# Kernel tuning notes

Measured on AMD Instinct MI355X. Metric: run time of the kernel, lower is better.

The kernel has to match this reference:

```python
import jax, jax.numpy as jnp
import numpy as np

FP16_MAX = 65504.0  # clamp_fp16 bound
GROUP = 64          # SVDQuant int4 group size along in_features


def _int4_quant_dequant(w):
    """Symmetric per-(out_channel, group) int4 fake-quant of a weight [out, in].
    Emulates the W4 weight numerics of SVDQW4A4Linear at the dequantized level."""
    o, i = w.shape
    wg = w.reshape(o, i // GROUP, GROUP)
    scale = np.max(np.abs(wg), axis=-1, keepdims=True) / 7.0
    scale = np.where(scale == 0.0, 1.0, scale)
    q = np.clip(np.round(wg / scale), -8, 7)
    return (q * scale).reshape(o, i).astype(np.float32)


def setup_inputs() -> dict:
    dim, hidden = 3072, 8192
    B, S = 2, 4096
    rng = np.random.default_rng(0)
    # fused [w1; w3] weight: [2*hidden, dim]; down proj w2: [dim, hidden]
    w13 = _int4_quant_dequant((rng.standard_normal((2 * hidden, dim)) * 0.02).astype(np.float32))
    w2 = _int4_quant_dequant((rng.standard_normal((dim, hidden)) * 0.02).astype(np.float32))
    key = jax.random.key(0)
    x = jax.random.normal(key, (B, S, dim), dtype=jnp.float32)
    return {"x": x, "w13": jnp.asarray(w13), "w2": jnp.asarray(w2)}


def reference(x, w13, w2):
    # fused gate/up projection: [B,S,dim] @ [2H,dim]^T -> [B,S,2H]
    h = jnp.einsum("bsd,hd->bsh", x, w13)
    # NOTE: original code does `x3, x1 = x.chunk(2, dim=-1)` -> first half is x3
    x3, x1 = jnp.split(h, 2, axis=-1)
    g = jnp.clip(jax.nn.silu(x1) * x3, -FP16_MAX, FP16_MAX)  # clamp_fp16
    # down projection: [B,S,H] @ [dim,H]^T -> [B,S,dim]
    return jnp.einsum("bsh,dh->bsd", g, w2)
```

## Files before the change

### kernel.cpp

```cpp
#include <hip/hip_runtime.h>
#include <hip/hip_bf16.h>


typedef __attribute__((ext_vector_type(8))) __bf16 bf16x8;
typedef __attribute__((ext_vector_type(4))) float f32x4;

#define GLD_LDS16(gptr, lptr)                                                        \
  __builtin_amdgcn_global_load_lds(                                                  \
      (const __attribute__((address_space(1))) void*)(gptr),                         \
      (__attribute__((address_space(3))) void*)(lptr), 16, 0, 0)

__device__ __forceinline__ __bf16 bfr(float f) {
  unsigned int u = __builtin_bit_cast(unsigned int, f);
  unsigned short r = (unsigned short)((u + 0x7FFFu + ((u >> 16) & 1u)) >> 16);
  return __builtin_bit_cast(__bf16, r);
}

__global__ __launch_bounds__(256)
void k_cvt(const float* __restrict__ src, unsigned short* __restrict__ dst, long n) {
  long i = ((long)blockIdx.x * 256 + threadIdx.x) * 8;
  const long stride = (long)gridDim.x * 256 * 8;
  for (; i < n; i += stride) {
    float4 f0 = *(const float4*)(src + i);
    float4 f1 = *(const float4*)(src + i + 4);
    bf16x8 o;
    o[0] = bfr(f0.x); o[1] = bfr(f0.y); o[2] = bfr(f0.z); o[3] = bfr(f0.w);
    o[4] = bfr(f1.x); o[5] = bfr(f1.y); o[6] = bfr(f1.z); o[7] = bfr(f1.w);
    *(bf16x8*)(dst + i) = o;
  }
}

__device__ __forceinline__ void stage_f32_tile(const float* __restrict__ src, int ld,
                                               unsigned short* __restrict__ lds, int t) {
  const int srow = t >> 3;
  const int sg = t & 7;
#pragma unroll
  for (int c = 0; c < 4; ++c) {
    const int row = c * 32 + srow;
    const float* p = src + (size_t)row * ld + sg * 8;
    float4 f0 = *(const float4*)p;
    float4 f1 = *(const float4*)(p + 4);
    bf16x8 o;
    o[0] = bfr(f0.x); o[1] = bfr(f0.y); o[2] = bfr(f0.z); o[3] = bfr(f0.w);
    o[4] = bfr(f1.x); o[5] = bfr(f1.y); o[6] = bfr(f1.z); o[7] = bfr(f1.w);
    *(bf16x8*)(lds + row * 64 + ((sg ^ (row & 7)) * 8)) = o;
  }
}

__global__ __launch_bounds__(256, 2)
void k_gateup_f(const unsigned short* __restrict__ X,
                const unsigned short* __restrict__ W13,
                __hip_bfloat16* __restrict__ G)
{
  constexpr int K = 3072;
  constexpr int LDG = 8192;
  __shared__ unsigned short As[128 * 64];
  __shared__ unsigned short B3s[128 * 64];
  __shared__ unsigned short B1s[128 * 64];

  const int t = threadIdx.x;
  const int lane = t & 63;
  const int wid = t >> 6;
  const int wm = wid >> 1, wn = wid & 1;
  const int l15 = lane & 15, lhi = lane >> 4;
  const int nb = blockIdx.x, mb = blockIdx.y;

  const int srow = t >> 3;
  const int scol = ((t & 7) ^ (srow & 7)) * 8;
  const unsigned short* xa  = X   + (size_t)(mb * 128 + srow) * K + scol;
  const unsigned short* wb3 = W13 + (size_t)(nb * 128 + srow) * K + scol;
  const unsigned short* wb1 = W13 + (size_t)(8192 + nb * 128 + srow) * K + scol;
  unsigned short* lA  = As  + t * 8;
  unsigned short* lB3 = B3s + t * 8;
  unsigned short* lB1 = B1s + t * 8;

  f32x4 acc3[4][4], acc1[4][4];
#pragma unroll
  for (int i = 0; i < 4; ++i)
#pragma unroll
    for (int j = 0; j < 4; ++j) {
      acc3[i][j] = (f32x4){0.f, 0.f, 0.f, 0.f};
      acc1[i][j] = (f32x4){0.f, 0.f, 0.f, 0.f};
    }
  const int sw = l15 & 7;

  for (int kt = 0; kt < K; kt += 64) {
    __syncthreads();
#pragma unroll
    for (int c = 0; c < 4; ++c) {
      GLD_LDS16(xa  + (size_t)(c * 32) * K + kt, lA  + c * 2048);
      GLD_LDS16(wb3 + (size_t)(c * 32) * K + kt, lB3 + c * 2048);
      GLD_LDS16(wb1 + (size_t)(c * 32) * K + kt, lB1 + c * 2048);
    }
    __syncthreads();
#pragma unroll
    for (int kk = 0; kk < 2; ++kk) {
      const int slot = (kk * 4 + lhi) ^ sw;
      bf16x8 av[4], bv3[4], bv1[4];
#pragma unroll
      for (int i = 0; i < 4; ++i) {
        av[i]  = *(const bf16x8*)(As  + (wm * 64 + i * 16 + l15) * 64 + slot * 8);
        bv3[i] = *(const bf16x8*)(B3s + (wn * 64 + i * 16 + l15) * 64 + slot * 8);
        bv1[i] = *(const bf16x8*)(B1s + (wn * 64 + i * 16 + l15) * 64 + slot * 8);
      }
#pragma unroll
      for (int i = 0; i < 4; ++i)
#pragma unroll
        for (int j = 0; j < 4; ++j) {
          acc3[i][j] = __builtin_amdgcn_mfma_f32_16x16x32_bf16(av[i], bv3[j], acc3[i][j], 0, 0, 0);
          acc1[i][j] = __builtin_amdgcn_mfma_f32_16x16x32_bf16(av[i], bv1[j], acc1[i][j], 0, 0, 0);
        }
    }
  }

  const int gr0 = mb * 128 + wm * 64;
  const int gc0 = nb * 128 + wn * 64;
#pragma unroll
  for (int i = 0; i < 4; ++i)
#pragma unroll
    for (int j = 0; j < 4; ++j)
#pragma unroll
      for (int r = 0; r < 4; ++r) {
        float h3 = acc3[i][j][r];
        float h1 = acc1[i][j][r];
        float s  = h1 / (1.f + __expf(-h1));
        float g  = fminf(fmaxf(s * h3, -65504.f), 65504.f);
        G[(size_t)(gr0 + i * 16 + lhi * 4 + r) * LDG + (gc0 + j * 16 + l15)] =
            __float2bfloat16(g);
      }
}

__global__ __launch_bounds__(256, 2)
void k_gateup_s(const float* __restrict__ X,
                const float* __restrict__ W13,
                __hip_bfloat16* __restrict__ G)
{
  constexpr int K = 3072;
  constexpr int LDG = 8192;
  __shared__ unsigned short As[128 * 64];
  __shared__ unsigned short B3s[128 * 64];
  __shared__ unsigned short B1s[128 * 64];

  const int t = threadIdx.x;
  const int lane = t & 63;
  const int wid = t >> 6;
  const int wm = wid >> 1, wn = wid & 1;
  const int l15 = lane & 15, lhi = lane >> 4;
  const int nb = blockIdx.x, mb = blockIdx.y;

  const float* xa  = X   + (size_t)(mb * 128) * K;
  const float* wb3 = W13 + (size_t)(nb * 128) * K;
  const float* wb1 = W13 + (size_t)(8192 + nb * 128) * K;

  f32x4 acc3[4][4], acc1[4][4];
#pragma unroll
  for (int i = 0; i < 4; ++i)
#pragma unroll
    for (int j = 0; j < 4; ++j) {
      acc3[i][j] = (f32x4){0.f, 0.f, 0.f, 0.f};
      acc1[i][j] = (f32x4){0.f, 0.f, 0.f, 0.f};
    }
  const int sw = l15 & 7;

  for (int kt = 0; kt < K; kt += 64) {
    __syncthreads();
    stage_f32_tile(xa  + kt, K, As,  t);
    stage_f32_tile(wb3 + kt, K, B3s, t);
    stage_f32_tile(wb1 + kt, K, B1s, t);
    __syncthreads();
#pragma unroll
    for (int kk = 0; kk < 2; ++kk) {
      const int slot = (kk * 4 + lhi) ^ sw;
      bf16x8 av[4], bv3[4], bv1[4];
#pragma unroll
      for (int i = 0; i < 4; ++i) {
        av[i]  = *(const bf16x8*)(As  + (wm * 64 + i * 16 + l15) * 64 + slot * 8);
        bv3[i] = *(const bf16x8*)(B3s + (wn * 64 + i * 16 + l15) * 64 + slot * 8);
        bv1[i] = *(const bf16x8*)(B1s + (wn * 64 + i * 16 + l15) * 64 + slot * 8);
      }
#pragma unroll
      for (int i = 0; i < 4; ++i)
#pragma unroll
        for (int j = 0; j < 4; ++j) {
          acc3[i][j] = __builtin_amdgcn_mfma_f32_16x16x32_bf16(av[i], bv3[j], acc3[i][j], 0, 0, 0);
          acc1[i][j] = __builtin_amdgcn_mfma_f32_16x16x32_bf16(av[i], bv1[j], acc1[i][j], 0, 0, 0);
        }
    }
  }

  const int gr0 = mb * 128 + wm * 64;
  const int gc0 = nb * 128 + wn * 64;
#pragma unroll
  for (int i = 0; i < 4; ++i)
#pragma unroll
    for (int j = 0; j < 4; ++j)
#pragma unroll
      for (int r = 0; r < 4; ++r) {
        float h3 = acc3[i][j][r];
        float h1 = acc1[i][j][r];
        float s  = h1 / (1.f + __expf(-h1));
        float g  = fminf(fmaxf(s * h3, -65504.f), 65504.f);
        G[(size_t)(gr0 + i * 16 + lhi * 4 + r) * LDG + (gc0 + j * 16 + l15)] =
            __float2bfloat16(g);
      }
}

__global__ __launch_bounds__(256, 2)
void k_down_f(const unsigned short* __restrict__ G,
              const unsigned short* __restrict__ W2,
              float* __restrict__ Out)
{
  constexpr int K = 8192;
  constexpr int LDO = 3072;
  __shared__ unsigned short As[128 * 64];
  __shared__ unsigned short Bs[128 * 64];

  const int t = threadIdx.x;
  const int lane = t & 63;
  const int wid = t >> 6;
  const int wm = wid >> 1, wn = wid & 1;
  const int l15 = lane & 15, lhi = lane >> 4;
  const int nb = blockIdx.x, mb = blockIdx.y;

  const int srow = t >> 3;
  const int scol = ((t & 7) ^ (srow & 7)) * 8;
  const unsigned short* ga = G  + (size_t)(mb * 128 + srow) * K + scol;
  const unsigned short* wb = W2 + (size_t)(nb * 128 + srow) * K + scol;
  unsigned short* lA = As + t * 8;
  unsigned short* lB = Bs + t * 8;

  f32x4 acc[4][4];
#pragma unroll
  for (int i = 0; i < 4; ++i)
#pragma unroll
    for (int j = 0; j < 4; ++j)
      acc[i][j] = (f32x4){0.f, 0.f, 0.f, 0.f};
  const int sw = l15 & 7;

  for (int kt = 0; kt < K; kt += 64) {
    __syncthreads();
#pragma unroll
    for (int c = 0; c < 4; ++c) {
      GLD_LDS16(ga + (size_t)(c * 32) * K + kt, lA + c * 2048);
      GLD_LDS16(wb + (size_t)(c * 32) * K + kt, lB + c * 2048);
    }
    __syncthreads();
#pragma unroll
    for (int kk = 0; kk < 2; ++kk) {
      const int slot = (kk * 4 + lhi) ^ sw;
      bf16x8 av[4], bv[4];
#pragma unroll
      for (int i = 0; i < 4; ++i) {
        av[i] = *(const bf16x8*)(As + (wm * 64 + i * 16 + l15) * 64 + slot * 8);
        bv[i] = *(const bf16x8*)(Bs + (wn * 64 + i * 16 + l15) * 64 + slot * 8);
      }
#pragma unroll
      for (int i = 0; i < 4; ++i)
#pragma unroll
        for (int j = 0; j < 4; ++j)
          acc[i][j] = __builtin_amdgcn_mfma_f32_16x16x32_bf16(av[i], bv[j], acc[i][j], 0, 0, 0);
    }
  }

  const int r0 = mb * 128 + wm * 64;
  const int c0 = nb * 128 + wn * 64;
#pragma unroll
  for (int i = 0; i < 4; ++i)
#pragma unroll
    for (int j = 0; j < 4; ++j)
#pragma unroll
      for (int r = 0; r < 4; ++r)
        Out[(size_t)(r0 + i * 16 + lhi * 4 + r) * LDO + (c0 + j * 16 + l15)] =
            acc[i][j][r];
}

__global__ __launch_bounds__(256, 2)
void k_down_s(const unsigned short* __restrict__ G,
              const float* __restrict__ W2,
              float* __restrict__ Out)
{
  constexpr int K = 8192;
  constexpr int LDO = 3072;
  __shared__ unsigned short As[128 * 64];
  __shared__ unsigned short Bs[128 * 64];

  const int t = threadIdx.x;
  const int lane = t & 63;
  const int wid = t >> 6;
  const int wm = wid >> 1, wn = wid & 1;
  const int l15 = lane & 15, lhi = lane >> 4;
  const int nb = blockIdx.x, mb = blockIdx.y;

  const int srow = t >> 3;
  const int scol = ((t & 7) ^ (srow & 7)) * 8;
  const unsigned short* ga = G + (size_t)(mb * 128 + srow) * K + scol;
  const float* wb = W2 + (size_t)(nb * 128) * K;
  unsigned short* lA = As + t * 8;

  f32x4 acc[4][4];
#pragma unroll
  for (int i = 0; i < 4; ++i)
#pragma unroll
    for (int j = 0; j < 4; ++j)
      acc[i][j] = (f32x4){0.f, 0.f, 0.f, 0.f};
  const int sw = l15 & 7;

  for (int kt = 0; kt < K; kt += 64) {
    __syncthreads();
#pragma unroll
    for (int c = 0; c < 4; ++c)
      GLD_LDS16(ga + (size_t)(c * 32) * K + kt, lA + c * 2048);
    stage_f32_tile(wb + kt, K, Bs, t);
    __syncthreads();
#pragma unroll
    for (int kk = 0; kk < 2; ++kk) {
      const int slot = (kk * 4 + lhi) ^ sw;
      bf16x8 av[4], bv[4];
#pragma unroll
      for (int i = 0; i < 4; ++i) {
        av[i] = *(const bf16x8*)(As + (wm * 64 + i * 16 + l15) * 64 + slot * 8);
        bv[i] = *(const bf16x8*)(Bs + (wn * 64 + i * 16 + l15) * 64 + slot * 8);
      }
#pragma unroll
      for (int i = 0; i < 4; ++i)
#pragma unroll
        for (int j = 0; j < 4; ++j)
          acc[i][j] = __builtin_amdgcn_mfma_f32_16x16x32_bf16(av[i], bv[j], acc[i][j], 0, 0, 0);
    }
  }

  const int r0 = mb * 128 + wm * 64;
  const int c0 = nb * 128 + wn * 64;
#pragma unroll
  for (int i = 0; i < 4; ++i)
#pragma unroll
    for (int j = 0; j < 4; ++j)
#pragma unroll
      for (int r = 0; r < 4; ++r)
        Out[(size_t)(r0 + i * 16 + lhi * 4 + r) * LDO + (c0 + j * 16 + l15)] =
            acc[i][j][r];
}

extern "C" void kernel_launch(void* const* d_in, const int* in_sizes, int n_in,
                              void* d_out, int out_size, void* d_ws, size_t ws_size,
                              hipStream_t stream) {
  const float* x   = (const float*)d_in[0];
  const float* w13 = (const float*)d_in[1];
  const float* w2  = (const float*)d_in[2];
  float* out = (float*)d_out;

  const long NX = 25165824L, NW13 = 50331648L, NW2 = 25165824L;
  const size_t XB = 50331648, W13B = 100663296, W2B = 50331648, GB = 134217728;

  if (ws_size >= XB + W13B + W2B + GB) {
    unsigned short* xb   = (unsigned short*)d_ws;
    unsigned short* w13b = (unsigned short*)((char*)d_ws + XB);
    unsigned short* w2b  = (unsigned short*)((char*)d_ws + XB + W13B);
    __hip_bfloat16* g    = (__hip_bfloat16*)((char*)d_ws + XB + W13B + W2B);
    k_cvt<<<2048, 256, 0, stream>>>(x,   xb,   NX);
    k_cvt<<<2048, 256, 0, stream>>>(w13, w13b, NW13);
    k_cvt<<<2048, 256, 0, stream>>>(w2,  w2b,  NW2);
    k_gateup_f<<<dim3(64, 64), dim3(256), 0, stream>>>(xb, w13b, (__hip_bfloat16*)g);
    k_down_f<<<dim3(24, 64), dim3(256), 0, stream>>>((const unsigned short*)g, w2b, out);
  } else {
    long mc = (long)(ws_size / (8192 * 2));
    mc -= mc % 128;
    if (mc > 8192) mc = 8192;
    if (mc < 128) mc = 128;
    for (long m0 = 0; m0 < 8192; m0 += mc) {
      long mrows = 8192 - m0 < mc ? 8192 - m0 : mc;
      __hip_bfloat16* g = (__hip_bfloat16*)d_ws;
      k_gateup_s<<<dim3(64, mrows / 128), dim3(256), 0, stream>>>(
          x + m0 * 3072, w13, g);
      k_down_s<<<dim3(24, mrows / 128), dim3(256), 0, stream>>>(
          (const unsigned short*)g, w2, out + m0 * 3072);
    }
  }
}
```

Measured before the change: 1.234 ms.

## Rewrite GEMM kernels with 256x128 tiles, double-buffered LDS prefetch, and block swizzle

Replaces both GEMM kernels with 512-thread, 8-wave versions that use 256x128 output tiles. Global-to-LDS loads are double-buffered two K-steps ahead, with finer-grained waitcnt and barriers so loads overlap the MFMA work. The kernels also add s_setprio around MFMA bursts and a block-index swizzle for L2 locality. The chunked fallback path for a small workspace is dropped, so the code now assumes a large workspace is always available.

```diff
diff --git a/kernel.cpp b/kernel.cpp
--- a/kernel.cpp
+++ b/kernel.cpp
@@ -9,6 +9,19 @@
   __builtin_amdgcn_global_load_lds(                                                  \
       (const __attribute__((address_space(1))) void*)(gptr),                         \
       (__attribute__((address_space(3))) void*)(lptr), 16, 0, 0)
+
+#define VMCNT(n) asm volatile("s_waitcnt vmcnt(" #n ")" ::: "memory")
+#define BAR_SYNC()                                          \
+  do {                                                      \
+    asm volatile("s_waitcnt lgkmcnt(0)" ::: "memory");      \
+    __builtin_amdgcn_s_barrier();                           \
+    asm volatile("" ::: "memory");                          \
+  } while (0)
+#define BAR_ONLY()                                          \
+  do {                                                      \
+    __builtin_amdgcn_s_barrier();                           \
+    asm volatile("" ::: "memory");                          \
+  } while (0)
 
 __device__ __forceinline__ __bf16 bfr(float f) {
   unsigned int u = __builtin_bit_cast(unsigned int, f);
@@ -30,315 +43,262 @@
   }
 }
 
-__device__ __forceinline__ void stage_f32_tile(const float* __restrict__ src, int ld,
-                                               unsigned short* __restrict__ lds, int t) {
-  const int srow = t >> 3;
-  const int sg = t & 7;
-#pragma unroll
-  for (int c = 0; c < 4; ++c) {
-    const int row = c * 32 + srow;
-    const float* p = src + (size_t)row * ld + sg * 8;
-    float4 f0 = *(const float4*)p;
-    float4 f1 = *(const float4*)(p + 4);
-    bf16x8 o;
-    o[0] = bfr(f0.x); o[1] = bfr(f0.y); o[2] = bfr(f0.z); o[3] = bfr(f0.w);
-    o[4] = bfr(f1.x); o[5] = bfr(f1.y); o[6] = bfr(f1.z); o[7] = bfr(f1.w);
-    *(bf16x8*)(lds + row * 64 + ((sg ^ (row & 7)) * 8)) = o;
-  }
-}
-
-__global__ __launch_bounds__(256, 2)
-void k_gateup_f(const unsigned short* __restrict__ X,
-                const unsigned short* __restrict__ W13,
-                __hip_bfloat16* __restrict__ G)
+__global__ __launch_bounds__(512, 2)
+void k_gateup8(const unsigned short* __restrict__ X,
+               const unsigned short* __restrict__ W13,
+               __hip_bfloat16* __restrict__ G)
 {
-  constexpr int K = 3072;
-  constexpr int LDG = 8192;
-  __shared__ unsigned short As[128 * 64];
-  __shared__ unsigned short B3s[128 * 64];
-  __shared__ unsigned short B1s[128 * 64];
+  constexpr int K = 3072, LDG = 8192, NT = K / 64;
+  __shared__ unsigned short lds[65536];
 
   const int t = threadIdx.x;
-  const int lane = t & 63;
-  const int wid = t >> 6;
-  const int wm = wid >> 1, wn = wid & 1;
-  const int l15 = lane & 15, lhi = lane >> 4;
-  const int nb = blockIdx.x, mb = blockIdx.y;
+  const int lane = t & 63, wid = t >> 6;
+  const int wm = wid >> 2, wn = wid & 3;
+  const int l15 = lane & 15, lhi = lane >> 4, sw = l15 & 7;
+
+  const int bid = blockIdx.x;
+  const int swz = (bid & 7) * 256 + (bid >> 3);
+  const int mb = swz >> 6, nb = swz & 63;
 
   const int srow = t >> 3;
   const int scol = ((t & 7) ^ (srow & 7)) * 8;
-  const unsigned short* xa  = X   + (size_t)(mb * 128 + srow) * K + scol;
-  const unsigned short* wb3 = W13 + (size_t)(nb * 128 + srow) * K + scol;
-  const unsigned short* wb1 = W13 + (size_t)(8192 + nb * 128 + srow) * K + scol;
-  unsigned short* lA  = As  + t * 8;
-  unsigned short* lB3 = B3s + t * 8;
-  unsigned short* lB1 = B1s + t * 8;
-
-  f32x4 acc3[4][4], acc1[4][4];
-#pragma unroll
-  for (int i = 0; i < 4; ++i)
-#pragma unroll
-    for (int j = 0; j < 4; ++j) {
-      acc3[i][j] = (f32x4){0.f, 0.f, 0.f, 0.f};
-      acc1[i][j] = (f32x4){0.f, 0.f, 0.f, 0.f};
-    }
-  const int sw = l15 & 7;
-
-  for (int kt = 0; kt < K; kt += 64) {
-    __syncthreads();
-#pragma unroll
-    for (int c = 0; c < 4; ++c) {
-      GLD_LDS16(xa  + (size_t)(c * 32) * K + kt, lA  + c * 2048);
-      GLD_LDS16(wb3 + (size_t)(c * 32) * K + kt, lB3 + c * 2048);
-      GLD_LDS16(wb1 + (size_t)(c * 32) * K + kt, lB1 + c * 2048);
-    }
-    __syncthreads();
+  const unsigned short* xa = X   + (size_t)(mb * 256 + srow) * K + scol;
+  const unsigned short* b3 = W13 + (size_t)(nb * 128 + srow) * K + scol;
+  const unsigned short* b1 = W13 + (size_t)(8192 + nb * 128 + srow) * K + scol;
+  const int lo = t * 8;
+
+  f32x4 acc3[8][2], acc1[8][2];
+#pragma unroll
+  for (int m = 0; m < 8; ++m)
+#pragma unroll
+    for (int n = 0; n < 2; ++n) {
+      acc3[m][n] = (f32x4){0.f, 0.f, 0.f, 0.f};
+      acc1[m][n] = (f32x4){0.f, 0.f, 0.f, 0.f};
+    }
+
+#pragma unroll
+  for (int tt = 0; tt < 2; ++tt) {
+    unsigned short* A  = lds + tt * 32768;
+    unsigned short* B3 = A + 16384;
+    unsigned short* B1 = A + 24576;
+    const int kt = tt * 64;
+#pragma unroll
+    for (int q = 0; q < 4; ++q)
+      GLD_LDS16(xa + (size_t)(q * 64) * K + kt, A + q * 4096 + lo);
+#pragma unroll
+    for (int r = 0; r < 2; ++r) {
+      GLD_LDS16(b3 + (size_t)(r * 64) * K + kt, B3 + r * 4096 + lo);
+      GLD_LDS16(b1 + (size_t)(r * 64) * K + kt, B1 + r * 4096 + lo);
+    }
+  }
+
+  for (int tk = 0; tk < NT; ++tk) {
+    unsigned short* A  = lds + (tk & 1) * 32768;
+    unsigned short* B3 = A + 16384;
+    unsigned short* B1 = A + 24576;
+    const int ks = (tk + 2 < NT ? tk + 2 : 0) * 64;
+
+    VMCNT(8);
+    BAR_ONLY();
+
+    bf16x8 ra[4][2], r3a[2], r1a[2], r3b[2], r1b[2];
+#pragma unroll
+    for (int m = 0; m < 4; ++m)
+#pragma unroll
+      for (int kk = 0; kk < 2; ++kk)
+        ra[m][kk] = *(const bf16x8*)(A + (wm * 128 + m * 16 + l15) * 64 + ((kk * 4 + lhi) ^ sw) * 8);
 #pragma unroll
     for (int kk = 0; kk < 2; ++kk) {
-      const int slot = (kk * 4 + lhi) ^ sw;
-      bf16x8 av[4], bv3[4], bv1[4];
-#pragma unroll
-      for (int i = 0; i < 4; ++i) {
-        av[i]  = *(const bf16x8*)(As  + (wm * 64 + i * 16 + l15) * 64 + slot * 8);
-        bv3[i] = *(const bf16x8*)(B3s + (wn * 64 + i * 16 + l15) * 64 + slot * 8);
-        bv1[i] = *(const bf16x8*)(B1s + (wn * 64 + i * 16 + l15) * 64 + slot * 8);
-      }
-#pragma unroll
-      for (int i = 0; i < 4; ++i)
-#pragma unroll
-        for (int j = 0; j < 4; ++j) {
-          acc3[i][j] = __builtin_amdgcn_mfma_f32_16x16x32_bf16(av[i], bv3[j], acc3[i][j], 0, 0, 0);
-          acc1[i][j] = __builtin_amdgcn_mfma_f32_16x16x32_bf16(av[i], bv1[j], acc1[i][j], 0, 0, 0);
-        }
-    }
-  }
-
-  const int gr0 = mb * 128 + wm * 64;
-  const int gc0 = nb * 128 + wn * 64;
-#pragma unroll
-  for (int i = 0; i < 4; ++i)
-#pragma unroll
-    for (int j = 0; j < 4; ++j)
+      r3a[kk] = *(const bf16x8*)(B3 + (wn * 32 + l15) * 64 + ((kk * 4 + lhi) ^ sw) * 8);
+      r1a[kk] = *(const bf16x8*)(B1 + (wn * 32 + l15) * 64 + ((kk * 4 + lhi) ^ sw) * 8);
+    }
+    __builtin_amdgcn_s_setprio(1);
+#pragma unroll
+    for (int m = 0; m < 4; ++m)
+#pragma unroll
+      for (int kk = 0; kk < 2; ++kk) {
+        acc3[m][0] = __builtin_amdgcn_mfma_f32_16x16x32_bf16(ra[m][kk], r3a[kk], acc3[m][0], 0, 0, 0);
+        acc1[m][0] = __builtin_amdgcn_mfma_f32_16x16x32_bf16(ra[m][kk], r1a[kk], acc1[m][0], 0, 0, 0);
+      }
+    __builtin_amdgcn_s_setprio(0);
+    BAR_SYNC();
+
+    GLD_LDS16(xa + (size_t)(0 * 64) * K + ks, A + 0 * 4096 + lo);
+    GLD_LDS16(xa + (size_t)(2 * 64) * K + ks, A + 2 * 4096 + lo);
+#pragma unroll
+    for (int kk = 0; kk < 2; ++kk) {
+      r3b[kk] = *(const bf16x8*)(B3 + (wn * 32 + 16 + l15) * 64 + ((kk * 4 + lhi) ^ sw) * 8);
+      r1b[kk] = *(const bf16x8*)(B1 + (wn * 32 + 16 + l15) * 64 + ((kk * 4 + lhi) ^ sw) * 8);
+    }
+    __builtin_amdgcn_s_setprio(1);
+#pragma unroll
+    for (int m = 0; m < 4; ++m)
+#pragma unroll
+      for (int kk = 0; kk < 2; ++kk) {
+        acc3[m][1] = __builtin_amdgcn_mfma_f32_16x16x32_bf16(ra[m][kk], r3b[kk], acc3[m][1], 0, 0, 0);
+        acc1[m][1] = __builtin_amdgcn_mfma_f32_16x16x32_bf16(ra[m][kk], r1b[kk], acc1[m][1], 0, 0, 0);
+      }
+    __builtin_amdgcn_s_setprio(0);
+    BAR_SYNC();
+
+#pragma unroll
+    for (int r = 0; r < 2; ++r) {
+      GLD_LDS16(b3 + (size_t)(r * 64) * K + ks, B3 + r * 4096 + lo);
+      GLD_LDS16(b1 + (size_t)(r * 64) * K + ks, B1 + r * 4096 + lo);
+    }
+#pragma unroll
+    for (int m = 0; m < 4; ++m)
+#pragma unroll
+      for (int kk = 0; kk < 2; ++kk)
+        ra[m][kk] = *(const bf16x8*)(A + (wm * 128 + 64 + m * 16 + l15) * 64 + ((kk * 4 + lhi) ^ sw) * 8);
+    __builtin_amdgcn_s_setprio(1);
+#pragma unroll
+    for (int m = 0; m < 4; ++m)
+#pragma unroll
+      for (int kk = 0; kk < 2; ++kk) {
+        acc3[4 + m][0] = __builtin_amdgcn_mfma_f32_16x16x32_bf16(ra[m][kk], r3a[kk], acc3[4 + m][0], 0, 0, 0);
+        acc1[4 + m][0] = __builtin_amdgcn_mfma_f32_16x16x32_bf16(ra[m][kk], r1a[kk], acc1[4 + m][0], 0, 0, 0);
+      }
+    __builtin_amdgcn_s_setprio(0);
+    BAR_SYNC();
+
+    GLD_LDS16(xa + (size_t)(1 * 64) * K + ks, A + 1 * 4096 + lo);
+    GLD_LDS16(xa + (size_t)(3 * 64) * K + ks, A + 3 * 4096 + lo);
+    __builtin_amdgcn_s_setprio(1);
+#pragma unroll
+    for (int m = 0; m < 4; ++m)
+#pragma unroll
+      for (int kk = 0; kk < 2; ++kk) {
+        acc3[4 + m][1] = __builtin_amdgcn_mfma_f32_16x16x32_bf16(ra[m][kk], r3b[kk], acc3[4 + m][1], 0, 0, 0);
+        acc1[4 + m][1] = __builtin_amdgcn_mfma_f32_16x16x32_bf16(ra[m][kk], r1b[kk], acc1[4 + m][1], 0, 0, 0);
+      }
+    __builtin_amdgcn_s_setprio(0);
+  }
+
+  const int gr0 = mb * 256 + wm * 128;
+  const int gc0 = nb * 128 + wn * 32;
+#pragma unroll
+  for (int m = 0; m < 8; ++m)
+#pragma unroll
+    for (int n = 0; n < 2; ++n)
 #pragma unroll
       for (int r = 0; r < 4; ++r) {
-        float h3 = acc3[i][j][r];
-        float h1 = acc1[i][j][r];
+        float h3 = acc3[m][n][r];
+        float h1 = acc1[m][n][r];
         float s  = h1 / (1.f + __expf(-h1));
         float g  = fminf(fmaxf(s * h3, -65504.f), 65504.f);
-        G[(size_t)(gr0 + i * 16 + lhi * 4 + r) * LDG + (gc0 + j * 16 + l15)] =
+        G[(size_t)(gr0 + m * 16 + lhi * 4 + r) * LDG + (gc0 + n * 16 + l15)] =
             __float2bfloat16(g);
       }
 }
 
-__global__ __launch_bounds__(256, 2)
-void k_gateup_s(const float* __restrict__ X,
-                const float* __restrict__ W13,
-                __hip_bfloat16* __restrict__ G)
+__global__ __launch_bounds__(512, 2)
+void k_down8(const unsigned short* __restrict__ Gm,
+             const unsigned short* __restrict__ W2,
+             float* __restrict__ Out)
 {
-  constexpr int K = 3072;
-  constexpr int LDG = 8192;
-  __shared__ unsigned short As[128 * 64];
-  __shared__ unsigned short B3s[128 * 64];
-  __shared__ unsigned short B1s[128 * 64];
+  constexpr int K = 8192, LDO = 3072, NT = K / 64;
+  __shared__ unsigned short lds[49152];
 
   const int t = threadIdx.x;
-  const int lane = t & 63;
-  const int wid = t >> 6;
-  const int wm = wid >> 1, wn = wid & 1;
-  const int l15 = lane & 15, lhi = lane >> 4;
-  const int nb = blockIdx.x, mb = blockIdx.y;
-
-  const float* xa  = X   + (size_t)(mb * 128) * K;
-  const float* wb3 = W13 + (size_t)(nb * 128) * K;
-  const float* wb1 = W13 + (size_t)(8192 + nb * 128) * K;
-
-  f32x4 acc3[4][4], acc1[4][4];
-#pragma unroll
-  for (int i = 0; i < 4; ++i)
-#pragma unroll
-    for (int j = 0; j < 4; ++j) {
-      acc3[i][j] = (f32x4){0.f, 0.f, 0.f, 0.f};
-      acc1[i][j] = (f32x4){0.f, 0.f, 0.f, 0.f};
-    }
-  const int sw = l15 & 7;
-
-  for (int kt = 0; kt < K; kt += 64) {
-    __syncthreads();
-    stage_f32_tile(xa  + kt, K, As,  t);
-    stage_f32_tile(wb3 + kt, K, B3s, t);
-    stage_f32_tile(wb1 + kt, K, B1s, t);
-    __syncthreads();
-#pragma unroll
-    for (int kk = 0; kk < 2; ++kk) {
-      const int slot = (kk * 4 + lhi) ^ sw;
-      bf16x8 av[4], bv3[4], bv1[4];
-#pragma unroll
-      for (int i = 0; i < 4; ++i) {
-        av[i]  = *(const bf16x8*)(As  + (wm * 64 + i * 16 + l15) * 64 + slot * 8);
-        bv3[i] = *(const bf16x8*)(B3s + (wn * 64 + i * 16 + l15) * 64 + slot * 8);
-        bv1[i] = *(const bf16x8*)(B1s + (wn * 64 + i * 16 + l15) * 64 + slot * 8);
-      }
-#pragma unroll
-      for (int i = 0; i < 4; ++i)
-#pragma unroll
-        for (int j = 0; j < 4; ++j) {
-          acc3[i][j] = __builtin_amdgcn_mfma_f32_16x16x32_bf16(av[i], bv3[j], acc3[i][j], 0, 0, 0);
-          acc1[i][j] = __builtin_amdgcn_mfma_f32_16x16x32_bf16(av[i], bv1[j], acc1[i][j], 0, 0, 0);
-        }
-    }
-  }
-
-  const int gr0 = mb * 128 + wm * 64;
-  const int gc0 = nb * 128 + wn * 64;
-#pragma unroll
-  for (int i = 0; i < 4; ++i)
-#pragma unroll
-    for (int j = 0; j < 4; ++j)
-#pragma unroll
-      for (int r = 0; r < 4; ++r) {
-        float h3 = acc3[i][j][r];
-        float h1 = acc1[i][j][r];
-        float s  = h1 / (1.f + __expf(-h1));
-        float g  = fminf(fmaxf(s * h3, -65504.f), 65504.f);
-        G[(size_t)(gr0 + i * 16 + lhi * 4 + r) * LDG + (gc0 + j * 16 + l15)] =
-            __float2bfloat16(g);
-      }
-}
-
-__global__ __launch_bounds__(256, 2)
-void k_down_f(const unsigned short* __restrict__ G,
-              const unsigned short* __restrict__ W2,
-              float* __restrict__ Out)
-{
-  constexpr int K = 8192;
-  constexpr int LDO = 3072;
-  __shared__ unsigned short As[128 * 64];
-  __shared__ unsigned short Bs[128 * 64];
-
-  const int t = threadIdx.x;
-  const int lane = t & 63;
-  const int wid = t >> 6;
-  const int wm = wid >> 1, wn = wid & 1;
-  const int l15 = lane & 15, lhi = lane >> 4;
-  const int nb = blockIdx.x, mb = blockIdx.y;
+  const int lane = t & 63, wid = t >> 6;
+  const int wm = wid >> 2, wn = wid & 3;
+  const int l15 = lane & 15, lhi = lane >> 4, sw = l15 & 7;
+
+  const int bid = blockIdx.x;
+  const int swz = (bid & 7) * 96 + (bid >> 3);
+  const int mb = swz / 24, nb = swz % 24;
 
   const int srow = t >> 3;
   const int scol = ((t & 7) ^ (srow & 7)) * 8;
-  const unsigned short* ga = G  + (size_t)(mb * 128 + srow) * K + scol;
+  const unsigned short* ga = Gm + (size_t)(mb * 256 + srow) * K + scol;
   const unsigned short* wb = W2 + (size_t)(nb * 128 + srow) * K + scol;
-  unsigned short* lA = As + t * 8;
-  unsigned short* lB = Bs + t * 8;
-
-  f32x4 acc[4][4];
-#pragma unroll
-  for (int i = 0; i < 4; ++i)
-#pragma unroll
-    for (int j = 0; j < 4; ++j)
-      acc[i][j] = (f32x4){0.f, 0.f, 0.f, 0.f};
-  const int sw = l15 & 7;
-
-  for (int kt = 0; kt < K; kt += 64) {
-    __syncthreads();
-#pragma unroll
-    for (int c = 0; c < 4; ++c) {
-      GLD_LDS16(ga + (size_t)(c * 32) * K + kt, lA + c * 2048);
-      GLD_LDS16(wb + (size_t)(c * 32) * K + kt, lB + c * 2048);
-    }
-    __syncthreads();
-#pragma unroll
-    for (int kk = 0; kk < 2; ++kk) {
-      const int slot = (kk * 4 + lhi) ^ sw;
-      bf16x8 av[4], bv[4];
-#pragma unroll
-      for (int i = 0; i < 4; ++i) {
-        av[i] = *(const bf16x8*)(As + (wm * 64 + i * 16 + l15) * 64 + slot * 8);
-        bv[i] = *(const bf16x8*)(Bs + (wn * 64 + i * 16 + l15) * 64 + slot * 8);
-      }
-#pragma unroll
-      for (int i = 0; i < 4; ++i)
-#pragma unroll
-        for (int j = 0; j < 4; ++j)
-          acc[i][j] = __builtin_amdgcn_mfma_f32_16x16x32_bf16(av[i], bv[j], acc[i][j], 0, 0, 0);
-    }
-  }
-
-  const int r0 = mb * 128 + wm * 64;
-  const int c0 = nb * 128 + wn * 64;
-#pragma unroll
-  for (int i = 0; i < 4; ++i)
-#pragma unroll
-    for (int j = 0; j < 4; ++j)
+  const int lo = t * 8;
+
+  f32x4 acc[8][2];
+#pragma unroll
+  for (int m = 0; m < 8; ++m)
+#pragma unroll
+    for (int n = 0; n < 2; ++n)
+      acc[m][n] = (f32x4){0.f, 0.f, 0.f, 0.f};
+
+#pragma unroll
+  for (int tt = 0; tt < 2; ++tt) {
+    unsigned short* A = lds + tt * 24576;
+    unsigned short* B = A + 16384;
+    const int kt = tt * 64;
+#pragma unroll
+    for (int q = 0; q < 4; ++q)
+      GLD_LDS16(ga + (size_t)(q * 64) * K + kt, A + q * 4096 + lo);
+#pragma unroll
+    for (int r = 0; r < 2; ++r)
+      GLD_LDS16(wb + (size_t)(r * 64) * K + kt, B + r * 4096 + lo);
+  }
+
+  for (int tk = 0; tk < NT; ++tk) {
+    unsigned short* A = lds + (tk & 1) * 24576;
+    unsigned short* B = A + 16384;
+    const int ks = (tk + 2 < NT ? tk + 2 : 0) * 64;
+
+    VMCNT(6);
+    BAR_ONLY();
+
+    bf16x8 ra[4][2], rb[2][2];
+#pragma unroll
+    for (int m = 0; m < 4; ++m)
+#pragma unroll
+      for (int kk = 0; kk < 2; ++kk)
+        ra[m][kk] = *(const bf16x8*)(A + (wm * 128 + m * 16 + l15) * 64 + ((kk * 4 + lhi) ^ sw) * 8);
+#pragma unroll
+    for (int n = 0; n < 2; ++n)
+#pragma unroll
+      for (int kk = 0; kk < 2; ++kk)
+        rb[n][kk] = *(const bf16x8*)(B + (wn * 32 + n * 16 + l15) * 64 + ((kk * 4 + lhi) ^ sw) * 8);
+    __builtin_amdgcn_s_setprio(1);
+#pragma unroll
+    for (int m = 0; m < 4; ++m)
+#pragma unroll
+      for (int n = 0; n < 2; ++n)
+#pragma unroll
+        for (int kk = 0; kk < 2; ++kk)
+          acc[m][n] = __builtin_amdgcn_mfma_f32_16x16x32_bf16(ra[m][kk], rb[n][kk], acc[m][n], 0, 0, 0);
+    __builtin_amdgcn_s_setprio(0);
+    BAR_SYNC();
+
+#pragma unroll
+    for (int r = 0; r < 2; ++r)
+      GLD_LDS16(wb + (size_t)(r * 64) * K + ks, B + r * 4096 + lo);
+    GLD_LDS16(ga + (size_t)(0 * 64) * K + ks, A + 0 * 4096 + lo);
+    GLD_LDS16(ga + (size_t)(2 * 64) * K + ks, A + 2 * 4096 + lo);
+#pragma unroll
+    for (int m = 0; m < 4; ++m)
+#pragma unroll
+      for (int kk = 0; kk < 2; ++kk)
+        ra[m][kk] = *(const bf16x8*)(A + (wm * 128 + 64 + m * 16 + l15) * 64 + ((kk * 4 + lhi) ^ sw) * 8);
+    __builtin_amdgcn_s_setprio(1);
+#pragma unroll
+    for (int m = 0; m < 4; ++m)
+#pragma unroll
+      for (int n = 0; n < 2; ++n)
+#pragma unroll
+        for (int kk = 0; kk < 2; ++kk)
+          acc[4 + m][n] = __builtin_amdgcn_mfma_f32_16x16x32_bf16(ra[m][kk], rb[n][kk], acc[4 + m][n], 0, 0, 0);
+    __builtin_amdgcn_s_setprio(0);
+    BAR_SYNC();
+    GLD_LDS16(ga + (size_t)(1 * 64) * K + ks, A + 1 * 4096 + lo);
+    GLD_LDS16(ga + (size_t)(3 * 64) * K + ks, A + 3 * 4096 + lo);
+  }
+
+  const int r0 = mb * 256 + wm * 128;
+  const int c0 = nb * 128 + wn * 32;
+#pragma unroll
+  for (int m = 0; m < 8; ++m)
+#pragma unroll
+    for (int n = 0; n < 2; ++n)
 #pragma unroll
       for (int r = 0; r < 4; ++r)
-        Out[(size_t)(r0 + i * 16 + lhi * 4 + r) * LDO + (c0 + j * 16 + l15)] =
-            acc[i][j][r];
-}
-
-__global__ __launch_bounds__(256, 2)
-void k_down_s(const unsigned short* __restrict__ G,
-              const float* __restrict__ W2,
-              float* __restrict__ Out)
-{
-  constexpr int K = 8192;
-  constexpr int LDO = 3072;
-  __shared__ unsigned short As[128 * 64];
-  __shared__ unsigned short Bs[128 * 64];
-
-  const int t = threadIdx.x;
-  const int lane = t & 63;
-  const int wid = t >> 6;
-  const int wm = wid >> 1, wn = wid & 1;
-  const int l15 = lane & 15, lhi = lane >> 4;
-  const int nb = blockIdx.x, mb = blockIdx.y;
-
-  const int srow = t >> 3;
-  const int scol = ((t & 7) ^ (srow & 7)) * 8;
-  const unsigned short* ga = G + (size_t)(mb * 128 + srow) * K + scol;
-  const float* wb = W2 + (size_t)(nb * 128) * K;
-  unsigned short* lA = As + t * 8;
-
-  f32x4 acc[4][4];
-#pragma unroll
-  for (int i = 0; i < 4; ++i)
-#pragma unroll
-    for (int j = 0; j < 4; ++j)
-      acc[i][j] = (f32x4){0.f, 0.f, 0.f, 0.f};
-  const int sw = l15 & 7;
-
-  for (int kt = 0; kt < K; kt += 64) {
-    __syncthreads();
-#pragma unroll
-    for (int c = 0; c < 4; ++c)
-      GLD_LDS16(ga + (size_t)(c * 32) * K + kt, lA + c * 2048);
-    stage_f32_tile(wb + kt, K, Bs, t);
-    __syncthreads();
-#pragma unroll
-    for (int kk = 0; kk < 2; ++kk) {
-      const int slot = (kk * 4 + lhi) ^ sw;
-      bf16x8 av[4], bv[4];
-#pragma unroll
-      for (int i = 0; i < 4; ++i) {
-        av[i] = *(const bf16x8*)(As + (wm * 64 + i * 16 + l15) * 64 + slot * 8);
-        bv[i] = *(const bf16x8*)(Bs + (wn * 64 + i * 16 + l15) * 64 + slot * 8);
-      }
-#pragma unroll
-      for (int i = 0; i < 4; ++i)
-#pragma unroll
-        for (int j = 0; j < 4; ++j)
-          acc[i][j] = __builtin_amdgcn_mfma_f32_16x16x32_bf16(av[i], bv[j], acc[i][j], 0, 0, 0);
-    }
-  }
-
-  const int r0 = mb * 128 + wm * 64;
-  const int c0 = nb * 128 + wn * 64;
-#pragma unroll
-  for (int i = 0; i < 4; ++i)
-#pragma unroll
-    for (int j = 0; j < 4; ++j)
-#pragma unroll
-      for (int r = 0; r < 4; ++r)
-        Out[(size_t)(r0 + i * 16 + lhi * 4 + r) * LDO + (c0 + j * 16 + l15)] =
-            acc[i][j][r];
+        Out[(size_t)(r0 + m * 16 + lhi * 4 + r) * LDO + (c0 + n * 16 + l15)] =
+            acc[m][n][r];
 }
 
 extern "C" void kernel_launch(void* const* d_in, const int* in_sizes, int n_in,
@@ -350,30 +310,16 @@
   float* out = (float*)d_out;
 
   const long NX = 25165824L, NW13 = 50331648L, NW2 = 25165824L;
-  const size_t XB = 50331648, W13B = 100663296, W2B = 50331648, GB = 134217728;
-
-  if (ws_size >= XB + W13B + W2B + GB) {
-    unsigned short* xb   = (unsigned short*)d_ws;
-    unsigned short* w13b = (unsigned short*)((char*)d_ws + XB);
-    unsigned short* w2b  = (unsigned short*)((char*)d_ws + XB + W13B);
-    __hip_bfloat16* g    = (__hip_bfloat16*)((char*)d_ws + XB + W13B + W2B);
-    k_cvt<<<2048, 256, 0, stream>>>(x,   xb,   NX);
-    k_cvt<<<2048, 256, 0, stream>>>(w13, w13b, NW13);
-    k_cvt<<<2048, 256, 0, stream>>>(w2,  w2b,  NW2);
-    k_gateup_f<<<dim3(64, 64), dim3(256), 0, stream>>>(xb, w13b, (__hip_bfloat16*)g);
-    k_down_f<<<dim3(24, 64), dim3(256), 0, stream>>>((const unsigned short*)g, w2b, out);
-  } else {
-    long mc = (long)(ws_size / (8192 * 2));
-    mc -= mc % 128;
-    if (mc > 8192) mc = 8192;
-    if (mc < 128) mc = 128;
-    for (long m0 = 0; m0 < 8192; m0 += mc) {
-      long mrows = 8192 - m0 < mc ? 8192 - m0 : mc;
-      __hip_bfloat16* g = (__hip_bfloat16*)d_ws;
-      k_gateup_s<<<dim3(64, mrows / 128), dim3(256), 0, stream>>>(
-          x + m0 * 3072, w13, g);
-      k_down_s<<<dim3(24, mrows / 128), dim3(256), 0, stream>>>(
-          (const unsigned short*)g, w2, out + m0 * 3072);
-    }
-  }
-}
+  const size_t XB = 50331648, W13B = 100663296, W2B = 50331648;
+
+  unsigned short* xb   = (unsigned short*)d_ws;
+  unsigned short* w13b = (unsigned short*)((char*)d_ws + XB);
+  unsigned short* w2b  = (unsigned short*)((char*)d_ws + XB + W13B);
+  __hip_bfloat16* g    = (__hip_bfloat16*)((char*)d_ws + XB + W13B + W2B);
+
+  k_cvt<<<2048, 256, 0, stream>>>(x,   xb,   NX);
+  k_cvt<<<2048, 256, 0, stream>>>(w13, w13b, NW13);
+  k_cvt<<<2048, 256, 0, stream>>>(w2,  w2b,  NW2);
+  k_gateup8<<<2048, 512, 0, stream>>>(xb, w13b, g);
+  k_down8<<<768, 512, 0, stream>>>((const unsigned short*)g, w2b, out);
+}
```

Result: faster. 1.200 ms (-2.8%).
